# Performance work log

Hardware: AMD Instinct MI355X
Metric: run time of the kernel (lower is better)

## Reference

```python
import jax, jax.numpy as jnp
import numpy as np

D = 768
NH = 12
HD = D // NH
N_MLP = 3072
LN_EPS = 1e-6


def layer_norm(x, g, b, eps=LN_EPS):
    mu = jnp.mean(x, axis=-1, keepdims=True)
    var = jnp.mean(jnp.square(x - mu), axis=-1, keepdims=True)
    return (x - mu) * jax.lax.rsqrt(var + eps) * g + b


def setup_inputs() -> dict:
    key = jax.random.key(0)
    ks = jax.random.split(key, 6)
    x = jax.random.normal(ks[0], (2, 4096, D), dtype=jnp.float32)
    # torch Linear weights are (out, in); init std=0.02, zero bias
    W_qkv = 0.02 * jax.random.normal(ks[1], (3 * D, D), dtype=jnp.float32)
    b_qkv = jnp.zeros((3 * D,), dtype=jnp.float32)
    W_proj = 0.02 * jax.random.normal(ks[2], (D, D), dtype=jnp.float32)
    b_proj = jnp.zeros((D,), dtype=jnp.float32)
    W1 = 0.02 * jax.random.normal(ks[3], (N_MLP, D), dtype=jnp.float32)
    b1 = jnp.zeros((N_MLP,), dtype=jnp.float32)
    W2 = 0.02 * jax.random.normal(ks[4], (D, N_MLP), dtype=jnp.float32)
    b2 = jnp.zeros((D,), dtype=jnp.float32)
    g1 = jnp.ones((D,), dtype=jnp.float32)
    beta1 = jnp.zeros((D,), dtype=jnp.float32)
    g2 = jnp.ones((D,), dtype=jnp.float32)
    beta2 = jnp.zeros((D,), dtype=jnp.float32)
    return dict(x=x, W_qkv=W_qkv, b_qkv=b_qkv, W_proj=W_proj, b_proj=b_proj,
                W1=W1, b1=b1, W2=W2, b2=b2,
                g1=g1, beta1=beta1, g2=g2, beta2=beta2)


def reference(x, W_qkv, b_qkv, W_proj, b_proj, W1, b1, W2, b2, g1, beta1, g2, beta2):
    B, T, d = x.shape
    scale = HD ** (-0.5)
    # --- attention branch (pre-norm) ---
    h = layer_norm(x, g1, beta1)
    qkv = h @ W_qkv.T + b_qkv                      # [B,T,3d]
    qkv = qkv.reshape(B, T, 3, NH, HD)
    q, k, v = qkv[:, :, 0], qkv[:, :, 1], qkv[:, :, 2]  # [B,T,NH,HD]
    logits = jnp.einsum('bthc,bshc->bhts', q, k) * scale
    attn = jax.nn.softmax(logits, axis=-1)
    out = jnp.einsum('bhts,bshc->bthc', attn, v).reshape(B, T, d)
    out = out @ W_proj.T + b_proj
    x = x + out
    # --- MLP branch (pre-norm) ---
    h = layer_norm(x, g2, beta2)
    h = jax.nn.gelu(h @ W1.T + b1, approximate=False)
    h = h @ W2.T + b2
    return x + h
```

## Files before the change

### kernel.cpp

```cpp
#include <hip/hip_runtime.h>
#include <cmath>

typedef __attribute__((ext_vector_type(4))) float f32x4;
typedef __attribute__((ext_vector_type(16))) float f32x16;
typedef __attribute__((ext_vector_type(8))) __bf16 bf16x8;
typedef __attribute__((ext_vector_type(8))) unsigned short u16x8;
typedef __attribute__((ext_vector_type(4))) unsigned short u16x4;
typedef __attribute__((ext_vector_type(2))) unsigned int u32x2;
typedef __attribute__((ext_vector_type(4))) unsigned int u32x4;

#define DEV __device__ __forceinline__

DEV unsigned short f2b(float v) {
  __bf16 b = (__bf16)v;
  return __builtin_bit_cast(unsigned short, b);
}

DEV unsigned int cvtpk(float lo, float hi) {
  unsigned int r;
  asm("v_cvt_pk_bf16_f32 %0, %1, %2" : "=v"(r) : "v"(lo), "v"(hi));
  return r;
}

DEV float exp2a(float x) {
  float r;
  asm("v_exp_f32 %0, %1" : "=v"(r) : "v"(x));
  return r;
}

DEV void swap32(unsigned int& x, unsigned int& y) {
  asm("v_permlane32_swap_b32 %0, %1" : "+v"(x), "+v"(y));
}

DEV u32x2 tr_b16(const unsigned short* p) {
  u32x2 r;
  asm volatile("ds_read_b64_tr_b16 %0, %1"
               : "=v"(r)
               : "v"((unsigned int)(unsigned long long)p)
               : "memory");
  return r;
}

DEV void gll16(const void* g, const void* l) {
  __builtin_amdgcn_global_load_lds(
      (const __attribute__((address_space(1))) unsigned int*)(unsigned long long)g,
      (__attribute__((address_space(3))) unsigned int*)(unsigned int)(unsigned long long)l,
      16, 0, 0);
}

__global__ void k_cvt_bf16(const float* __restrict__ src,
                           unsigned short* __restrict__ dst, int n4) {
  int i = blockIdx.x * blockDim.x + threadIdx.x;
  if (i >= n4) return;
  float4 v = ((const float4*)src)[i];
  u16x4 o = {f2b(v.x), f2b(v.y), f2b(v.z), f2b(v.w)};
  *(u16x4*)(dst + (size_t)i * 4) = o;
}

__global__ void k_ln(const float* __restrict__ x, const float* __restrict__ g,
                     const float* __restrict__ be, unsigned short* __restrict__ out) {
  int row = blockIdx.x;
  int l = threadIdx.x;
  const float* xr = x + (size_t)row * 768;
  float4 v[3];
  float s = 0.f, sq = 0.f;
#pragma unroll
  for (int j = 0; j < 3; ++j) {
    v[j] = ((const float4*)xr)[l + 64 * j];
    s += v[j].x + v[j].y + v[j].z + v[j].w;
    sq += v[j].x * v[j].x + v[j].y * v[j].y + v[j].z * v[j].z + v[j].w * v[j].w;
  }
#pragma unroll
  for (int m = 1; m < 64; m <<= 1) {
    s += __shfl_xor(s, m);
    sq += __shfl_xor(sq, m);
  }
  float mu = s * (1.f / 768.f);
  float var = sq * (1.f / 768.f) - mu * mu;
  float rs = rsqrtf(var + 1e-6f);
  unsigned short* orow = out + (size_t)row * 768;
#pragma unroll
  for (int j = 0; j < 3; ++j) {
    int c4 = l + 64 * j;
    float4 gv = ((const float4*)g)[c4];
    float4 bv = ((const float4*)be)[c4];
    u16x4 o = {f2b((v[j].x - mu) * rs * gv.x + bv.x),
               f2b((v[j].y - mu) * rs * gv.y + bv.y),
               f2b((v[j].z - mu) * rs * gv.z + bv.z),
               f2b((v[j].w - mu) * rs * gv.w + bv.w)};
    *(u16x4*)(orow + c4 * 4) = o;
  }
}

template <int MODE, int BM>
__global__ __launch_bounds__(256, 2) void k_gemm(
    const unsigned short* __restrict__ A, const unsigned short* __restrict__ Bw,
    const float* __restrict__ bias, const float* __restrict__ res,
    void* __restrict__ outp, int N, int K) {
  __shared__ unsigned short As[2][BM * 32];
  __shared__ unsigned short Bs[2][128 * 32];
  constexpr int MR = BM / 32;
  constexpr int AI = BM / 64;
  const int tid = threadIdx.x;
  const int w = tid >> 6, l = tid & 63;
  const int wr = w >> 1, wc = w & 1;
  const int lr = l & 15, lg = l >> 4;
  const int nwg = gridDim.x * gridDim.y;
  const int bid = blockIdx.y * gridDim.x + blockIdx.x;
  const int swz = (bid & 7) * (nwg >> 3) + (bid >> 3);
  const int bx = swz % gridDim.x, by = swz / gridDim.x;
  const int brow = by * BM, bcol = bx * 128;

  auto stage = [&](int buf, int kt) {
#pragma unroll
    for (int i = 0; i < AI; ++i) {
      int c = i * 256 + tid;
      int row = c >> 2, cg = (c & 3) ^ (row & 3);
      gll16(A + (size_t)(brow + row) * K + kt + cg * 8,
            (const char*)As[buf] + (i * 256 + (w << 6)) * 16);
    }
#pragma unroll
    for (int i = 0; i < 2; ++i) {
      int c = i * 256 + tid;
      int row = c >> 2, cg = (c & 3) ^ (row & 3);
      gll16(Bw + (size_t)(bcol + row) * K + kt + cg * 8,
            (const char*)Bs[buf] + (i * 256 + (w << 6)) * 16);
    }
  };

  stage(0, 0);
  f32x4 acc[MR][4] = {};
  int buf = 0;
  for (int kt = 0; kt < K; kt += 32, buf ^= 1) {
    asm volatile("s_waitcnt vmcnt(0)" ::: "memory");
    __syncthreads();
    if (kt + 32 < K) stage(buf ^ 1, kt + 32);
    bf16x8 af[MR], bfr[4];
#pragma unroll
    for (int m = 0; m < MR; ++m) {
      int row = wr * (BM / 2) + m * 16 + lr;
      af[m] = *(const bf16x8*)&As[buf][row * 32 + ((lg ^ (row & 3)) << 3)];
    }
#pragma unroll
    for (int n = 0; n < 4; ++n) {
      int row = wc * 64 + n * 16 + lr;
      bfr[n] = *(const bf16x8*)&Bs[buf][row * 32 + ((lg ^ (row & 3)) << 3)];
    }
#pragma unroll
    for (int m = 0; m < MR; ++m)
#pragma unroll
      for (int n = 0; n < 4; ++n)
        acc[m][n] = __builtin_amdgcn_mfma_f32_16x16x32_bf16(af[m], bfr[n], acc[m][n], 0, 0, 0);
  }
#pragma unroll
  for (int n = 0; n < 4; ++n) {
    int col = bcol + wc * 64 + n * 16 + lr;
    float bv = bias[col];
#pragma unroll
    for (int m = 0; m < MR; ++m) {
      int row0 = brow + wr * (BM / 2) + m * 16 + lg * 4;
#pragma unroll
      for (int r = 0; r < 4; ++r) {
        size_t idx = (size_t)(row0 + r) * N + col;
        float v = acc[m][n][r] + bv;
        if (MODE == 0) {
          ((unsigned short*)outp)[idx] = f2b(v);
        } else if (MODE == 1) {
          ((float*)outp)[idx] = v + res[idx];
        } else if (MODE == 2) {
          ((unsigned short*)outp)[idx] = f2b(0.5f * v * (1.f + erff(v * 0.70710678f)));
        } else {
          ((float*)outp)[idx] = v + res[idx];
        }
      }
    }
  }
}

__global__ __launch_bounds__(256, 4) void k_attn(const unsigned short* __restrict__ qkv,
                                                 f32x4* __restrict__ Opart,
                                                 float* __restrict__ ml) {
  __shared__ unsigned short Ks[2][64 * 64];
  __shared__ unsigned short Vs[2][4 * 64 * 16];
  const int tid = threadIdx.x;
  const int w = tid >> 6, l = tid & 63;
  const int lq = l & 31, hi = l >> 5;
  const int p = blockIdx.x;
  const int linear = (p & 7) * 192 + (p >> 3);
  const int bh = linear >> 6, rem = linear & 63;
  const int qt = rem >> 1, half = rem & 1;
  const int b = bh / 12, h = bh % 12;
  const size_t base = (size_t)b * 4096 * 2304;
  const int qbase = qt * 128 + w * 32;
  const int kv0 = half * 2048;

  const float SC = 0.18033688f;
  bf16x8 qb[4];
#pragma unroll
  for (int s = 0; s < 4; ++s) {
    u16x8 raw = *(const u16x8*)(qkv + base + (size_t)(qbase + lq) * 2304 + h * 64 +
                                s * 16 + hi * 8);
    u32x4 pk;
#pragma unroll
    for (int d = 0; d < 4; ++d) {
      float f0 = __builtin_bit_cast(float, (unsigned int)raw[2 * d] << 16) * SC;
      float f1 = __builtin_bit_cast(float, (unsigned int)raw[2 * d + 1] << 16) * SC;
      pk[d] = cvtpk(f0, f1);
    }
    qb[s] = __builtin_bit_cast(bf16x8, pk);
  }

  const unsigned short* pK = qkv + base + (size_t)(kv0 + 16 * w + (l >> 3)) * 2304 + 768 +
                             h * 64 + (((l & 7) ^ ((l >> 3) & 7)) << 3);
  const unsigned short* pV = qkv + base + (size_t)(kv0 + (l >> 1)) * 2304 + 1536 + h * 64 +
                             w * 16 + ((l & 1) << 3);
  const size_t STEP = (size_t)64 * 2304;

  {
    const char* dK = (const char*)&Ks[0][0] + w * 2048;
    const char* dV = (const char*)&Vs[0][0] + w * 2048;
    gll16(pK, dK);
    gll16(pK + 8 * 2304, dK + 1024);
    gll16(pV, dV);
    gll16(pV + 32 * 2304, dV + 1024);
    pK += STEP;
    pV += STEP;
  }

  f32x16 O[2] = {};
  float lrun = 0.f;

  int it = 0;
  for (int t = 0; t < 32; ++t, it ^= 1) {
    asm volatile("s_waitcnt vmcnt(0)" ::: "memory");
    __syncthreads();
    if (t < 31) {
      const char* dK = (const char*)&Ks[it ^ 1][0] + w * 2048;
      const char* dV = (const char*)&Vs[it ^ 1][0] + w * 2048;
      gll16(pK, dK);
      gll16(pK + 8 * 2304, dK + 1024);
      gll16(pV, dV);
      gll16(pV + 32 * 2304, dV + 1024);
      pK += STEP;
      pV += STEP;
    }

    f32x16 st[2] = {{0}, {0}};
    __builtin_amdgcn_s_setprio(1);
#pragma unroll
    for (int kt = 0; kt < 2; ++kt) {
      int key = kt * 32 + lq;
#pragma unroll
      for (int s = 0; s < 4; ++s) {
        bf16x8 ka =
            *(const bf16x8*)&Ks[it][key * 64 + ((s * 16 + hi * 8) ^ ((key & 7) << 3))];
        st[kt] = __builtin_amdgcn_mfma_f32_32x32x16_bf16(ka, qb[s], st[kt], 0, 0, 0);
      }
    }
    __builtin_amdgcn_s_setprio(0);

    float s0 = 0.f, s1 = 0.f, s2 = 0.f, s3 = 0.f;
#pragma unroll
    for (int kt = 0; kt < 2; ++kt) {
#pragma unroll
      for (int r = 0; r < 16; r += 4) {
        float p0 = exp2a(st[kt][r + 0]);
        float p1 = exp2a(st[kt][r + 1]);
        float p2 = exp2a(st[kt][r + 2]);
        float p3 = exp2a(st[kt][r + 3]);
        st[kt][r + 0] = p0;
        st[kt][r + 1] = p1;
        st[kt][r + 2] = p2;
        st[kt][r + 3] = p3;
        s0 += p0;
        s1 += p1;
        s2 += p2;
        s3 += p3;
      }
    }
    float ssum = (s0 + s1) + (s2 + s3);
    lrun += ssum + __shfl_xor(ssum, 32);

    u32x4 pf[4];
#pragma unroll
    for (int kt = 0; kt < 2; ++kt)
#pragma unroll
      for (int h2 = 0; h2 < 2; ++h2) {
        int r0 = h2 * 8;
        unsigned int a0 = cvtpk(st[kt][r0 + 0], st[kt][r0 + 1]);
        unsigned int a1 = cvtpk(st[kt][r0 + 2], st[kt][r0 + 3]);
        unsigned int b0 = cvtpk(st[kt][r0 + 4], st[kt][r0 + 5]);
        unsigned int b1 = cvtpk(st[kt][r0 + 6], st[kt][r0 + 7]);
        swap32(a0, b0);
        swap32(a1, b1);
        pf[kt * 2 + h2] = u32x4{a0, a1, b0, b1};
      }

#pragma unroll
    for (int hb = 0; hb < 2; ++hb) {
      u32x2 vt[4][2];
      const unsigned short* vbase = &Vs[it][(hb * 2 + (lq >> 4)) * 1024 + (lq & 15)];
#pragma unroll
      for (int s = 0; s < 4; ++s)
#pragma unroll
        for (int t2 = 0; t2 < 2; ++t2)
          vt[s][t2] = tr_b16(vbase + ((s * 16 + hi * 8 + t2 * 4) << 4));
      asm volatile("s_waitcnt lgkmcnt(0)" ::: "memory");
      __builtin_amdgcn_sched_barrier(0);
      __builtin_amdgcn_s_setprio(1);
#pragma unroll
      for (int s = 0; s < 4; ++s) {
        u32x4 vv = {vt[s][0].x, vt[s][0].y, vt[s][1].x, vt[s][1].y};
        O[hb] = __builtin_amdgcn_mfma_f32_32x32x16_bf16(
            __builtin_bit_cast(bf16x8, vv), __builtin_bit_cast(bf16x8, pf[s]), O[hb], 0, 0, 0);
      }
      __builtin_amdgcn_s_setprio(0);
    }
  }

  if (hi == 0) ml[(linear * 4 + w) * 32 + lq] = lrun;
#pragma unroll
  for (int hb = 0; hb < 2; ++hb)
#pragma unroll
    for (int g = 0; g < 4; ++g) {
      int k = hb * 4 + g;
      f32x4 v = {O[hb][4 * g + 0], O[hb][4 * g + 1], O[hb][4 * g + 2], O[hb][4 * g + 3]};
      Opart[((linear * 4 + w) * 8 + k) * 64 + l] = v;
    }
}

__global__ __launch_bounds__(256) void k_merge(const f32x4* __restrict__ Opart,
                                               const float* __restrict__ ml,
                                               unsigned short* __restrict__ out) {
  const int g = blockIdx.x;
  const int bh = g >> 5, qt = g & 31;
  const int b = bh / 12, h = bh % 12;
  const int tid = threadIdx.x;
  const int w = tid >> 6, l = tid & 63;
  const int lq = l & 31, hi = l >> 5;
  const int bidA = bh * 64 + qt * 2;
  const int bidB = bidA + 1;
  float l0 = ml[(bidA * 4 + w) * 32 + lq];
  float l1 = ml[(bidB * 4 + w) * 32 + lq];
  float rl = 1.f / (l0 + l1);
  const int t = qt * 128 + w * 32 + lq;
  unsigned short* orow = out + (size_t)(b * 4096 + t) * 768 + h * 64;
#pragma unroll
  for (int hb = 0; hb < 2; ++hb)
#pragma unroll
    for (int gg = 0; gg < 4; ++gg) {
      int k = hb * 4 + gg;
      f32x4 va = Opart[((bidA * 4 + w) * 8 + k) * 64 + l];
      f32x4 vb = Opart[((bidB * 4 + w) * 8 + k) * 64 + l];
      f32x4 v = (va + vb) * rl;
      unsigned int d0 = cvtpk(v[0], v[1]);
      unsigned int d1 = cvtpk(v[2], v[3]);
      *(u32x2*)(orow + hb * 32 + 8 * gg + 4 * hi) = u32x2{d0, d1};
    }
}

extern "C" void kernel_launch(void* const* d_in, const int* in_sizes, int n_in,
                              void* d_out, int out_size, void* d_ws, size_t ws_size,
                              hipStream_t stream) {
  const float* x = (const float*)d_in[0];
  const float* Wqkv = (const float*)d_in[1];
  const float* bqkv = (const float*)d_in[2];
  const float* Wproj = (const float*)d_in[3];
  const float* bproj = (const float*)d_in[4];
  const float* W1 = (const float*)d_in[5];
  const float* b1 = (const float*)d_in[6];
  const float* W2 = (const float*)d_in[7];
  const float* b2 = (const float*)d_in[8];
  const float* g1 = (const float*)d_in[9];
  const float* be1 = (const float*)d_in[10];
  const float* g2 = (const float*)d_in[11];
  const float* be2 = (const float*)d_in[12];

  char* ws = (char*)d_ws;
  unsigned short* wqkv = (unsigned short*)(ws + 0);
  unsigned short* wproj = (unsigned short*)(ws + 3538944);
  unsigned short* ww1 = (unsigned short*)(ws + 4718592);
  unsigned short* ww2 = (unsigned short*)(ws + 9437184);
  unsigned short* h1 = (unsigned short*)(ws + 14155776);
  unsigned short* qkvb = (unsigned short*)(ws + 26738688);
  unsigned short* attno = (unsigned short*)(ws + 64487424);
  float* x1 = (float*)(ws + 77070336);
  unsigned short* h2 = (unsigned short*)(ws + 102236160);
  unsigned short* m1 = (unsigned short*)(ws + 114819072);
  f32x4* Opart = (f32x4*)m1;
  float* mlbuf = (float*)h1;

  k_cvt_bf16<<<1728, 256, 0, stream>>>(Wqkv, wqkv, 442368);
  k_cvt_bf16<<<576, 256, 0, stream>>>(Wproj, wproj, 147456);
  k_cvt_bf16<<<2304, 256, 0, stream>>>(W1, ww1, 589824);
  k_cvt_bf16<<<2304, 256, 0, stream>>>(W2, ww2, 589824);

  k_ln<<<8192, 64, 0, stream>>>(x, g1, be1, h1);
  k_gemm<0, 128><<<dim3(18, 64), 256, 0, stream>>>(h1, wqkv, bqkv, nullptr, qkvb, 2304, 768);
  k_attn<<<1536, 256, 0, stream>>>(qkvb, Opart, mlbuf);
  k_merge<<<768, 256, 0, stream>>>(Opart, mlbuf, attno);
  k_gemm<1, 64><<<dim3(6, 128), 256, 0, stream>>>(attno, wproj, bproj, x, x1, 768, 768);
  k_ln<<<8192, 64, 0, stream>>>(x1, g2, be2, h2);
  k_gemm<2, 128><<<dim3(24, 64), 256, 0, stream>>>(h2, ww1, b1, nullptr, m1, 3072, 768);
  k_gemm<3, 64><<<dim3(6, 128), 256, 0, stream>>>(m1, ww2, b2, x1, (float*)d_out, 768, 3072);
}
```

Baseline: 369.2 us.

## Triple-buffer GEMM LDS staging with partial vmcnt waits

Result: faster. 356.2 us (-3.5%).

```diff
diff --git a/kernel.cpp b/kernel.cpp
--- a/kernel.cpp
+++ b/kernel.cpp
@@ -97,10 +97,11 @@
     const unsigned short* __restrict__ A, const unsigned short* __restrict__ Bw,
     const float* __restrict__ bias, const float* __restrict__ res,
     void* __restrict__ outp, int N, int K) {
-  __shared__ unsigned short As[2][BM * 32];
-  __shared__ unsigned short Bs[2][128 * 32];
+  __shared__ unsigned short As[3][BM * 32];
+  __shared__ unsigned short Bs[3][128 * 32];
   constexpr int MR = BM / 32;
   constexpr int AI = BM / 64;
+  constexpr int LPT = AI + 2;
   const int tid = threadIdx.x;
   const int w = tid >> 6, l = tid & 63;
   const int wr = w >> 1, wc = w & 1;
@@ -117,40 +118,53 @@
       int c = i * 256 + tid;
       int row = c >> 2, cg = (c & 3) ^ (row & 3);
       gll16(A + (size_t)(brow + row) * K + kt + cg * 8,
-            (const char*)As[buf] + (i * 256 + (w << 6)) * 16);
+            (const char*)&As[buf][0] + (i * 256 + (w << 6)) * 16);
     }
 #pragma unroll
     for (int i = 0; i < 2; ++i) {
       int c = i * 256 + tid;
       int row = c >> 2, cg = (c & 3) ^ (row & 3);
       gll16(Bw + (size_t)(bcol + row) * K + kt + cg * 8,
-            (const char*)Bs[buf] + (i * 256 + (w << 6)) * 16);
+            (const char*)&Bs[buf][0] + (i * 256 + (w << 6)) * 16);
     }
   };
 
   stage(0, 0);
+  if (32 < K) stage(1, 32);
   f32x4 acc[MR][4] = {};
-  int buf = 0;
-  for (int kt = 0; kt < K; kt += 32, buf ^= 1) {
-    asm volatile("s_waitcnt vmcnt(0)" ::: "memory");
-    __syncthreads();
-    if (kt + 32 < K) stage(buf ^ 1, kt + 32);
+  int cur = 0, nxt2 = 2;
+  for (int kt = 0; kt < K; kt += 32) {
+    if (kt + 32 < K) {
+      if constexpr (LPT == 4)
+        asm volatile("s_waitcnt vmcnt(4)" ::: "memory");
+      else
+        asm volatile("s_waitcnt vmcnt(3)" ::: "memory");
+    } else {
+      asm volatile("s_waitcnt vmcnt(0)" ::: "memory");
+    }
+    __builtin_amdgcn_s_barrier();
+    __builtin_amdgcn_sched_barrier(0);
+    if (kt + 64 < K) {
+      stage(nxt2, kt + 64);
+      nxt2 = (nxt2 == 2) ? 0 : nxt2 + 1;
+    }
     bf16x8 af[MR], bfr[4];
 #pragma unroll
     for (int m = 0; m < MR; ++m) {
       int row = wr * (BM / 2) + m * 16 + lr;
-      af[m] = *(const bf16x8*)&As[buf][row * 32 + ((lg ^ (row & 3)) << 3)];
+      af[m] = *(const bf16x8*)&As[cur][row * 32 + ((lg ^ (row & 3)) << 3)];
     }
 #pragma unroll
     for (int n = 0; n < 4; ++n) {
       int row = wc * 64 + n * 16 + lr;
-      bfr[n] = *(const bf16x8*)&Bs[buf][row * 32 + ((lg ^ (row & 3)) << 3)];
+      bfr[n] = *(const bf16x8*)&Bs[cur][row * 32 + ((lg ^ (row & 3)) << 3)];
     }
 #pragma unroll
     for (int m = 0; m < MR; ++m)
 #pragma unroll
       for (int n = 0; n < 4; ++n)
         acc[m][n] = __builtin_amdgcn_mfma_f32_16x16x32_bf16(af[m], bfr[n], acc[m][n], 0, 0, 0);
+    cur = (cur == 2) ? 0 : cur + 1;
   }
 #pragma unroll
   for (int n = 0; n < 4; ++n) {
```
